# Performance work log

Measured on AMD Instinct MI355X. Metric: run time of the kernel, lower is better.

The kernel has to match this reference:

```python
import jax, jax.numpy as jnp
import numpy as np
from jax import lax

B, N, C = 8, 100000, 90
H = W = 512
CONF_THR = 0.25
IOU_THR = 0.45
MAX_DET = 100  # fixed-size padded replacement for dynamic per-image NMS output


def setup_inputs() -> dict:
    key = jax.random.key(0)
    k1, k2, k3, k4, k5 = jax.random.split(key, 5)
    # small deltas so exp(dw), exp(dh) stay sane
    regression = jax.random.normal(k1, (B, N, 4), jnp.float32) * 0.1
    # shifted logits so sigmoid scores are mostly below conf_threshold (realistic sparsity)
    classification = jax.random.normal(k2, (B, N, C), jnp.float32) * 2.0 - 4.0
    # anchors in (y1, x1, y2, x2), valid boxes inside a 512x512 canvas
    cy = jax.random.uniform(k3, (1, N), minval=0.0, maxval=float(H))
    cx = jax.random.uniform(k4, (1, N), minval=0.0, maxval=float(W))
    hw = jax.random.uniform(k5, (1, N, 2), minval=16.0, maxval=128.0)
    hh, ww = hw[..., 0], hw[..., 1]
    anchors = jnp.stack([cy - hh / 2, cx - ww / 2, cy + hh / 2, cx + ww / 2], axis=-1)
    imgs = jnp.zeros((B, 3, H, W), jnp.float32)  # only shape (H, W) is used
    return {"regression": regression, "classification": classification,
            "anchors": anchors, "imgs": imgs}


def _bbox_transform(anchors, regression):
    y_c_a = (anchors[..., 0] + anchors[..., 2]) / 2
    x_c_a = (anchors[..., 1] + anchors[..., 3]) / 2
    ha = anchors[..., 2] - anchors[..., 0]
    wa = anchors[..., 3] - anchors[..., 1]
    w = jnp.exp(regression[..., 3]) * wa
    h = jnp.exp(regression[..., 2]) * ha
    y_c = regression[..., 0] * ha + y_c_a
    x_c = regression[..., 1] * wa + x_c_a
    # output in (x1, y1, x2, y2)
    return jnp.stack([x_c - w / 2, y_c - h / 2, x_c + w / 2, y_c + h / 2], axis=-1)


def _clip_boxes(boxes, height, width):
    x = jnp.clip(boxes[..., 0::2], 0.0, float(width))
    y = jnp.clip(boxes[..., 1::2], 0.0, float(height))
    return jnp.stack([x[..., 0], y[..., 0], x[..., 1], y[..., 1]], axis=-1)


def _iou_one_vs_all(box, boxes):
    # box [4], boxes [N,4] in x1y1x2y2
    x1 = jnp.maximum(box[0], boxes[:, 0])
    y1 = jnp.maximum(box[1], boxes[:, 1])
    x2 = jnp.minimum(box[2], boxes[:, 2])
    y2 = jnp.minimum(box[3], boxes[:, 3])
    inter = jnp.clip(x2 - x1, 0.0) * jnp.clip(y2 - y1, 0.0)
    area = (box[2] - box[0]) * (box[3] - box[1])
    areas = (boxes[:, 2] - boxes[:, 0]) * (boxes[:, 3] - boxes[:, 1])
    return inter / (area + areas - inter + 1e-8)


def _process_image(boxes, cls_logits):
    # boxes [N,4], cls_logits [N,C]
    scores_all = jax.nn.sigmoid(cls_logits)
    max_scores = jnp.max(scores_all, axis=1)
    labels = jnp.argmax(scores_all, axis=1)
    # below-threshold anchors get -1 so they can never be selected (== torch pre-NMS filter)
    s0 = jnp.where(max_scores > CONF_THR, max_scores, -1.0)
    s0 = lax.stop_gradient(s0)
    boxes_sg = lax.stop_gradient(boxes)

    def step(sc, _):
        best = jnp.argmax(sc)
        valid = sc[best] > 0.0
        iou = _iou_one_vs_all(boxes_sg[best], boxes_sg)
        sc = jnp.where(valid & (iou > IOU_THR), -1.0, sc)
        sc = sc.at[best].set(-1.0)
        return sc, jnp.where(valid, best, -1)

    _, idx = lax.scan(step, s0, None, length=MAX_DET)  # [MAX_DET] int
    valid = idx >= 0
    idx_safe = jnp.maximum(idx, 0)
    out_scores = jnp.where(valid, max_scores[idx_safe], 0.0)
    out_labels = jnp.where(valid, labels[idx_safe], -1)
    out_boxes = jnp.where(valid[:, None], boxes[idx_safe], 0.0)
    return out_scores, out_labels, out_boxes


def reference(regression, classification, anchors, imgs):
    height, width = imgs.shape[2], imgs.shape[3]
    boxes = _bbox_transform(anchors, regression)          # [B,N,4]
    boxes = _clip_boxes(boxes, height, width)
    scores, labels, det_boxes = jax.vmap(_process_image)(boxes, classification)
    # padded outputs: scores [B,MAX_DET], labels [B,MAX_DET] (-1 = invalid), boxes [B,MAX_DET,4]
    return scores, labels, det_boxes
```

## Files before the change

### kernel.cpp

```cpp
#include <hip/hip_runtime.h>

#define NB 8
#define NA 100000
#define NC 90
#define MAXDET 100
#define KCAND 2048
#define NBINS 4096
#define NBLK 13
#define BLK_ANCH 8000
#define ABLK 64
#define MASK_WORDS 32
#define SROWS 504
#define CONF 0.25f
#define IOUT 0.45f

static constexpr size_t OFF_SCORE = 0;
static constexpr size_t OFF_LABEL = OFF_SCORE + (size_t)NB * NA * 4;
static constexpr size_t OFF_HROWS = OFF_LABEL + (size_t)NB * NA;
static constexpr size_t OFF_THR   = OFF_HROWS + (size_t)NB * NBLK * NBINS * 4;
static constexpr size_t OFF_CNT   = OFF_THR + 64;
static constexpr size_t OFF_CKEY  = OFF_CNT + 64;
static constexpr size_t OFF_SSC   = OFF_CKEY + (size_t)NB * KCAND * 8;
static constexpr size_t OFF_SLAB  = OFF_SSC + (size_t)NB * KCAND * 4;
static constexpr size_t OFF_SBOX  = OFF_SLAB + (size_t)NB * KCAND * 4;
static constexpr size_t OFF_MASK  = OFF_SBOX + (size_t)NB * KCAND * 16;

__device__ __forceinline__ float4 decode_clip(float4 a, float4 r) {
#pragma clang fp contract(off)
    float yca = (a.x + a.z) * 0.5f;
    float xca = (a.y + a.w) * 0.5f;
    float ha  = a.z - a.x;
    float wa  = a.w - a.y;
    float w   = expf(r.w) * wa;
    float h   = expf(r.z) * ha;
    float yc  = r.x * ha + yca;
    float xc  = r.y * wa + xca;
    float x1  = xc - w * 0.5f, y1 = yc - h * 0.5f;
    float x2  = xc + w * 0.5f, y2 = yc + h * 0.5f;
    x1 = fminf(fmaxf(x1, 0.0f), 512.0f);
    x2 = fminf(fmaxf(x2, 0.0f), 512.0f);
    y1 = fminf(fmaxf(y1, 0.0f), 512.0f);
    y2 = fminf(fmaxf(y2, 0.0f), 512.0f);
    return make_float4(x1, y1, x2, y2);
}

__global__ __launch_bounds__(256) void k_score_box(const float* __restrict__ cls,
                                                   float* __restrict__ ws_score,
                                                   unsigned char* __restrict__ ws_label) {
    __shared__ float tile[ABLK * NC];
    int t = threadIdx.x;
    const float4* g4 = (const float4*)(cls + (size_t)blockIdx.x * (ABLK * NC));
    float4* t4 = (float4*)tile;
#pragma unroll
    for (int i = t; i < ABLK * NC / 4; i += 256) t4[i] = g4[i];
    __syncthreads();

    int la = t >> 2, h = t & 3;
    int off = h * 22 + (h < 2 ? h : 2);
    int len = (h < 2) ? 23 : 22;
    const float* row = tile + la * NC + off;
    unsigned bord = 0u;
    int bci = 0;
    for (int i = 0; i < len; ++i) {
        unsigned u = __float_as_uint(row[i]);
        unsigned ord = u ^ (0x80000000u | (unsigned)((int)u >> 31));
        if (ord > bord) { bord = ord; bci = off + i; }
    }
    unsigned long long best =
        ((unsigned long long)bord << 32) | (unsigned long long)(unsigned)(NC - 1 - bci);
    unsigned long long o = __shfl_xor(best, 1, 64);
    if (o > best) best = o;
    o = __shfl_xor(best, 2, 64);
    if (o > best) best = o;
    if (h == 0) {
        int a = blockIdx.x * ABLK + la;
        unsigned ordv = (unsigned)(best >> 32);
        unsigned u = (ordv & 0x80000000u) ? (ordv ^ 0x80000000u) : ~ordv;
        float x = __uint_as_float(u);
        float s = 1.0f / (1.0f + expf(-x));
        ws_score[a] = s;
        ws_label[a] = (unsigned char)(NC - 1 - (unsigned)(best & 0xFFFFFFFFu));
    }
}

__global__ __launch_bounds__(256) void k_hist(const float* __restrict__ ws_score,
                                              unsigned* __restrict__ hrows) {
    __shared__ unsigned h[NBINS];
    int b = blockIdx.y, blk = blockIdx.x, tid = threadIdx.x;
    for (int i = tid; i < NBINS; i += 256) h[i] = 0u;
    __syncthreads();
    int base = blk * BLK_ANCH;
    int lim = min(BLK_ANCH, NA - base);
    const float* sc = ws_score + (size_t)b * NA + base;
    for (int i = tid; i < lim; i += 256) {
        float s = sc[i];
        if (s > CONF) {
            int bin = min((int)(s * (float)NBINS), NBINS - 1);
            atomicAdd(&h[bin], 1u);
        }
    }
    __syncthreads();
    unsigned* row = hrows + ((size_t)b * NBLK + blk) * NBINS;
    for (int i = tid; i < NBINS; i += 256) row[i] = h[i];
}

__global__ __launch_bounds__(256) void k_thresh(const unsigned* __restrict__ hrows,
                                                unsigned* __restrict__ thr_bin,
                                                unsigned* __restrict__ cnt) {
    __shared__ unsigned h[NBINS];
    __shared__ unsigned chunk[256];
    __shared__ int bstar;
    int b = blockIdx.x, t = threadIdx.x;
    for (int i = t; i < NBINS; i += 256) {
        unsigned s = 0;
        for (int r = 0; r < NBLK; ++r) s += hrows[((size_t)b * NBLK + r) * NBINS + i];
        h[i] = s;
    }
    if (t == 0) { bstar = NBINS - 1; cnt[b] = 0u; }
    __syncthreads();
    unsigned s = 0;
    for (int j = 0; j < 16; ++j) s += h[t * 16 + j];
    chunk[t] = s;
    __syncthreads();
    unsigned U = 0;
    for (int j = t + 1; j < 256; ++j) U += chunk[j];
    unsigned run = U;
    int cand = NBINS;
    for (int j = 15; j >= 0; --j) {
        run += h[t * 16 + j];
        if (run <= (unsigned)KCAND) cand = t * 16 + j;
    }
    if (cand < NBINS) atomicMin(&bstar, cand);
    __syncthreads();
    if (t == 0) thr_bin[b] = (unsigned)bstar;
}

__global__ __launch_bounds__(256) void k_compact(const float* __restrict__ ws_score,
                                                 const unsigned* __restrict__ thr_bin,
                                                 unsigned* __restrict__ cnt,
                                                 unsigned long long* __restrict__ ckey) {
    __shared__ unsigned scan[256];
    __shared__ unsigned base_s;
    int b = blockIdx.y, blk = blockIdx.x, t = threadIdx.x;
    int base = blk * BLK_ANCH;
    int lim = min(BLK_ANCH, NA - base);
    size_t ibase = (size_t)b * NA + base;
    unsigned thr = thr_bin[b];

    unsigned c = 0;
    for (int i = t; i < lim; i += 256) {
        float s = ws_score[ibase + i];
        if (s > CONF) {
            int bin = min((int)(s * (float)NBINS), NBINS - 1);
            if ((unsigned)bin >= thr) c++;
        }
    }
    scan[t] = c;
    __syncthreads();
    for (int off = 1; off < 256; off <<= 1) {
        unsigned v = (t >= off) ? scan[t - off] : 0u;
        __syncthreads();
        scan[t] += v;
        __syncthreads();
    }
    if (t == 255) base_s = atomicAdd(&cnt[b], scan[255]);
    __syncthreads();
    unsigned pos = base_s + scan[t] - c;
    for (int i = t; i < lim; i += 256) {
        float s = ws_score[ibase + i];
        if (s > CONF) {
            int bin = min((int)(s * (float)NBINS), NBINS - 1);
            if ((unsigned)bin >= thr) {
                unsigned p = pos++;
                if (p < (unsigned)KCAND) {
                    int n = base + i;
                    ckey[(size_t)b * KCAND + p] =
                        ((unsigned long long)__float_as_uint(s) << 32) |
                        (unsigned long long)(0xFFFFFFFFu - (unsigned)n);
                }
            }
        }
    }
}

__global__ __launch_bounds__(1024) void k_sortdecode(const unsigned long long* __restrict__ ckey,
                                                     const unsigned* __restrict__ cnt,
                                                     const unsigned char* __restrict__ ws_label,
                                                     const float* __restrict__ reg,
                                                     const float* __restrict__ anc,
                                                     float* __restrict__ sscore,
                                                     int* __restrict__ slab,
                                                     float4* __restrict__ sbox) {
    __shared__ unsigned long long key[KCAND];
    int b = blockIdx.x, t = threadIdx.x;
    unsigned M = min(cnt[b], (unsigned)KCAND);
    for (int i = t; i < KCAND; i += 1024)
        key[i] = (i < (int)M) ? ckey[(size_t)b * KCAND + i] : 0ULL;
    __syncthreads();
    for (int k = 2; k <= KCAND; k <<= 1) {
        for (int j = k >> 1; j > 0; j >>= 1) {
#pragma unroll
            for (int s = 0; s < KCAND / 1024; ++s) {
                int p = t + s * 1024;
                int q = p ^ j;
                if (q > p) {
                    unsigned long long a = key[p], bb = key[q];
                    bool desc = ((p & k) == 0);
                    if (desc ? (a < bb) : (a > bb)) { key[p] = bb; key[q] = a; }
                }
            }
            __syncthreads();
        }
    }
    for (int i = t; i < KCAND; i += 1024) {
        unsigned long long kk = key[i];
        size_t o = (size_t)b * KCAND + i;
        if (kk != 0ULL) {
            unsigned n = 0xFFFFFFFFu - (unsigned)(kk & 0xFFFFFFFFu);
            sscore[o] = __uint_as_float((unsigned)(kk >> 32));
            slab[o] = (int)ws_label[(size_t)b * NA + n];
            float4 a4 = ((const float4*)anc)[n];
            float4 r4 = ((const float4*)reg)[(size_t)b * NA + n];
            sbox[o] = decode_clip(a4, r4);
        } else {
            sscore[o] = 0.0f;
            slab[o] = -1;
            sbox[o] = make_float4(0.f, 0.f, 0.f, 0.f);
        }
    }
}

__global__ __launch_bounds__(256) void k_mask(const float4* __restrict__ sbox,
                                              unsigned long long* __restrict__ mask) {
    __shared__ float4 bx[KCAND];
    int b = blockIdx.y, t = threadIdx.x;
    for (int i = t; i < KCAND; i += 256) bx[i] = sbox[(size_t)b * KCAND + i];
    __syncthreads();
    int r = t >> 5, w = t & 31;
    int row = blockIdx.x * 8 + r;
    float4 rb = bx[row];
    unsigned long long bits = 0ULL;
    {
#pragma clang fp contract(off)
        float areaR = (rb.z - rb.x) * (rb.w - rb.y);
        int cbase = w * 64;
        for (int cc = 0; cc < 64; ++cc) {
            float4 cb = bx[cbase + cc];
            float x1 = fmaxf(rb.x, cb.x), y1 = fmaxf(rb.y, cb.y);
            float x2 = fminf(rb.z, cb.z), y2 = fminf(rb.w, cb.w);
            float inter = fmaxf(x2 - x1, 0.0f) * fmaxf(y2 - y1, 0.0f);
            float areaC = (cb.z - cb.x) * (cb.w - cb.y);
            float iou = inter / (areaR + areaC - inter + 1e-8f);
            if (iou > IOUT) bits |= (1ULL << cc);
        }
    }
    mask[((size_t)b * KCAND + row) * MASK_WORDS + w] = bits;
}

__global__ __launch_bounds__(256) void k_scan(const unsigned long long* __restrict__ mask,
                                              const unsigned* __restrict__ cnt,
                                              const float* __restrict__ sscore,
                                              const int* __restrict__ slab,
                                              const float4* __restrict__ sbox,
                                              float* __restrict__ out) {
    __shared__ unsigned long long lmask[SROWS * MASK_WORDS];
    __shared__ int picks[MAXDET];
    __shared__ int np_s;
    int b = blockIdx.x, t = threadIdx.x;
    const unsigned long long* mb = mask + (size_t)b * KCAND * MASK_WORDS;

    float4* l4 = (float4*)lmask;
    const float4* m4 = (const float4*)mb;
    for (int i = t; i < SROWS * MASK_WORDS / 2; i += 256) l4[i] = m4[i];
    __syncthreads();

    if (t < 64) {
        int l = t;
        unsigned M = min(cnt[b], (unsigned)KCAND);
        unsigned long long valid = 0ULL;
        if (l < 32) {
            int rem = (int)M - l * 64;
            valid = (rem >= 64) ? ~0ULL : ((rem > 0) ? ((1ULL << rem) - 1ULL) : 0ULL);
        }
        unsigned long long removed = 0ULL;
        int np = 0;
        while (np < MAXDET) {
            unsigned long long free_ = valid & ~removed;
            unsigned long long act = __ballot(free_ != 0ULL);
            if (act == 0ULL) break;
            int lstar = __ffsll((long long)act) - 1;
            unsigned long long fw = __shfl(free_, lstar, 64);
            int bit = __ffsll((long long)fw) - 1;
            int c = lstar * 64 + bit;
            if (l == 0) picks[np] = c;
            np++;
            if (l == lstar) removed |= (1ULL << bit);
            if (l < 32) {
                unsigned long long rw;
                if (c < SROWS) rw = lmask[c * MASK_WORDS + l];
                else rw = mb[(size_t)c * MASK_WORDS + l];
                removed |= rw;
            }
        }
        if (l == 0) np_s = np;
    }
    __syncthreads();

    int np = np_s;
    for (int k = t; k < MAXDET; k += 256) {
        float sc = 0.0f, lb = -1.0f;
        float4 bb = make_float4(0.f, 0.f, 0.f, 0.f);
        if (k < np) {
            int i = picks[k];
            size_t o = (size_t)b * KCAND + i;
            sc = sscore[o];
            lb = (float)slab[o];
            bb = sbox[o];
        }
        out[b * MAXDET + k] = sc;
        out[NB * MAXDET + b * MAXDET + k] = lb;
        ((float4*)(out + 2 * NB * MAXDET))[b * MAXDET + k] = bb;
    }
}

extern "C" void kernel_launch(void* const* d_in, const int* in_sizes, int n_in,
                              void* d_out, int out_size, void* d_ws, size_t ws_size,
                              hipStream_t stream) {
    const float* reg = (const float*)d_in[0];
    const float* cls = (const float*)d_in[1];
    const float* anc = (const float*)d_in[2];

    char* ws = (char*)d_ws;
    float* ws_score           = (float*)(ws + OFF_SCORE);
    unsigned char* ws_label   = (unsigned char*)(ws + OFF_LABEL);
    unsigned* hrows           = (unsigned*)(ws + OFF_HROWS);
    unsigned* thr_bin         = (unsigned*)(ws + OFF_THR);
    unsigned* cnt             = (unsigned*)(ws + OFF_CNT);
    unsigned long long* ckey  = (unsigned long long*)(ws + OFF_CKEY);
    float* sscore             = (float*)(ws + OFF_SSC);
    int* slab                 = (int*)(ws + OFF_SLAB);
    float4* sbox              = (float4*)(ws + OFF_SBOX);
    unsigned long long* maskp = (unsigned long long*)(ws + OFF_MASK);

    float* out = (float*)d_out;

    k_score_box<<<NB * NA / ABLK, 256, 0, stream>>>(cls, ws_score, ws_label);
    k_hist<<<dim3(NBLK, NB), 256, 0, stream>>>(ws_score, hrows);
    k_thresh<<<NB, 256, 0, stream>>>(hrows, thr_bin, cnt);
    k_compact<<<dim3(NBLK, NB), 256, 0, stream>>>(ws_score, thr_bin, cnt, ckey);
    k_sortdecode<<<NB, 1024, 0, stream>>>(ckey, cnt, ws_label, reg, anc, sscore, slab, sbox);
    k_mask<<<dim3(KCAND / 8, NB), 256, 0, stream>>>(sbox, maskp);
    k_scan<<<NB, 256, 0, stream>>>(maskp, cnt, sscore, slab, sbox, out);
}
```

Before: 566.3 us.

## Fuse histogram, threshold and compaction into one per-image select kernel; skip lower-triangle mask

Replaces the three kernels for histogram, threshold and compaction with a single 1024-thread block per image. That block builds the histogram in shared memory, finds the threshold bin and compacts candidates in order without global atomics. This removes two launches and the global histogram round-trip, but the pass over 100k scores is now done by only 8 blocks. The mask kernel also remaps threads so each row skips 64-column words that lie entirely below the diagonal, and it rotates the column start to spread LDS bank accesses. Skipped words are written as zero, which assumes the scan only reads bits above the diagonal.

```diff
diff --git a/kernel.cpp b/kernel.cpp
--- a/kernel.cpp
+++ b/kernel.cpp
@@ -6,8 +6,6 @@
 #define MAXDET 100
 #define KCAND 2048
 #define NBINS 4096
-#define NBLK 13
-#define BLK_ANCH 8000
 #define ABLK 64
 #define MASK_WORDS 32
 #define SROWS 504
@@ -16,8 +14,7 @@
 
 static constexpr size_t OFF_SCORE = 0;
 static constexpr size_t OFF_LABEL = OFF_SCORE + (size_t)NB * NA * 4;
-static constexpr size_t OFF_HROWS = OFF_LABEL + (size_t)NB * NA;
-static constexpr size_t OFF_THR   = OFF_HROWS + (size_t)NB * NBLK * NBINS * 4;
+static constexpr size_t OFF_THR   = OFF_LABEL + (size_t)NB * NA;
 static constexpr size_t OFF_CNT   = OFF_THR + 64;
 static constexpr size_t OFF_CKEY  = OFF_CNT + 64;
 static constexpr size_t OFF_SSC   = OFF_CKEY + (size_t)NB * KCAND * 8;
@@ -83,104 +80,78 @@
     }
 }
 
-__global__ __launch_bounds__(256) void k_hist(const float* __restrict__ ws_score,
-                                              unsigned* __restrict__ hrows) {
-    __shared__ unsigned h[NBINS];
-    int b = blockIdx.y, blk = blockIdx.x, tid = threadIdx.x;
-    for (int i = tid; i < NBINS; i += 256) h[i] = 0u;
-    __syncthreads();
-    int base = blk * BLK_ANCH;
-    int lim = min(BLK_ANCH, NA - base);
-    const float* sc = ws_score + (size_t)b * NA + base;
-    for (int i = tid; i < lim; i += 256) {
+__global__ __launch_bounds__(1024) void k_select(const float* __restrict__ ws_score,
+                                                 unsigned* __restrict__ cnt,
+                                                 unsigned long long* __restrict__ ckey) {
+    __shared__ unsigned hist[NBINS];
+    __shared__ unsigned chunk[256];
+    __shared__ unsigned sscan[1024];
+    __shared__ int bstar;
+    int b = blockIdx.x, t = threadIdx.x;
+    const float* sc = ws_score + (size_t)b * NA;
+
+    for (int i = t; i < NBINS; i += 1024) hist[i] = 0u;
+    if (t == 0) bstar = NBINS - 1;
+    __syncthreads();
+    for (int i = t; i < NA; i += 1024) {
         float s = sc[i];
         if (s > CONF) {
             int bin = min((int)(s * (float)NBINS), NBINS - 1);
-            atomicAdd(&h[bin], 1u);
-        }
-    }
-    __syncthreads();
-    unsigned* row = hrows + ((size_t)b * NBLK + blk) * NBINS;
-    for (int i = tid; i < NBINS; i += 256) row[i] = h[i];
-}
-
-__global__ __launch_bounds__(256) void k_thresh(const unsigned* __restrict__ hrows,
-                                                unsigned* __restrict__ thr_bin,
-                                                unsigned* __restrict__ cnt) {
-    __shared__ unsigned h[NBINS];
-    __shared__ unsigned chunk[256];
-    __shared__ int bstar;
-    int b = blockIdx.x, t = threadIdx.x;
-    for (int i = t; i < NBINS; i += 256) {
+            atomicAdd(&hist[bin], 1u);
+        }
+    }
+    __syncthreads();
+    if (t < 256) {
         unsigned s = 0;
-        for (int r = 0; r < NBLK; ++r) s += hrows[((size_t)b * NBLK + r) * NBINS + i];
-        h[i] = s;
-    }
-    if (t == 0) { bstar = NBINS - 1; cnt[b] = 0u; }
-    __syncthreads();
-    unsigned s = 0;
-    for (int j = 0; j < 16; ++j) s += h[t * 16 + j];
-    chunk[t] = s;
-    __syncthreads();
-    unsigned U = 0;
-    for (int j = t + 1; j < 256; ++j) U += chunk[j];
-    unsigned run = U;
-    int cand = NBINS;
-    for (int j = 15; j >= 0; --j) {
-        run += h[t * 16 + j];
-        if (run <= (unsigned)KCAND) cand = t * 16 + j;
-    }
-    if (cand < NBINS) atomicMin(&bstar, cand);
-    __syncthreads();
-    if (t == 0) thr_bin[b] = (unsigned)bstar;
-}
-
-__global__ __launch_bounds__(256) void k_compact(const float* __restrict__ ws_score,
-                                                 const unsigned* __restrict__ thr_bin,
-                                                 unsigned* __restrict__ cnt,
-                                                 unsigned long long* __restrict__ ckey) {
-    __shared__ unsigned scan[256];
-    __shared__ unsigned base_s;
-    int b = blockIdx.y, blk = blockIdx.x, t = threadIdx.x;
-    int base = blk * BLK_ANCH;
-    int lim = min(BLK_ANCH, NA - base);
-    size_t ibase = (size_t)b * NA + base;
-    unsigned thr = thr_bin[b];
+        for (int j = 0; j < 16; ++j) s += hist[t * 16 + j];
+        chunk[t] = s;
+    }
+    __syncthreads();
+    if (t < 256) {
+        unsigned U = 0;
+        for (int j = t + 1; j < 256; ++j) U += chunk[j];
+        unsigned run = U;
+        int cand = NBINS;
+        for (int j = 15; j >= 0; --j) {
+            run += hist[t * 16 + j];
+            if (run <= (unsigned)KCAND) cand = t * 16 + j;
+        }
+        if (cand < NBINS) atomicMin(&bstar, cand);
+    }
+    __syncthreads();
+    unsigned thr = (unsigned)bstar;
 
     unsigned c = 0;
-    for (int i = t; i < lim; i += 256) {
-        float s = ws_score[ibase + i];
+    for (int i = t; i < NA; i += 1024) {
+        float s = sc[i];
         if (s > CONF) {
             int bin = min((int)(s * (float)NBINS), NBINS - 1);
             if ((unsigned)bin >= thr) c++;
         }
     }
-    scan[t] = c;
-    __syncthreads();
-    for (int off = 1; off < 256; off <<= 1) {
-        unsigned v = (t >= off) ? scan[t - off] : 0u;
+    sscan[t] = c;
+    __syncthreads();
+    for (int off = 1; off < 1024; off <<= 1) {
+        unsigned v = (t >= off) ? sscan[t - off] : 0u;
         __syncthreads();
-        scan[t] += v;
+        sscan[t] += v;
         __syncthreads();
     }
-    if (t == 255) base_s = atomicAdd(&cnt[b], scan[255]);
-    __syncthreads();
-    unsigned pos = base_s + scan[t] - c;
-    for (int i = t; i < lim; i += 256) {
-        float s = ws_score[ibase + i];
+    unsigned pos = sscan[t] - c;
+    for (int i = t; i < NA; i += 1024) {
+        float s = sc[i];
         if (s > CONF) {
             int bin = min((int)(s * (float)NBINS), NBINS - 1);
             if ((unsigned)bin >= thr) {
                 unsigned p = pos++;
-                if (p < (unsigned)KCAND) {
-                    int n = base + i;
+                if (p < (unsigned)KCAND)
                     ckey[(size_t)b * KCAND + p] =
                         ((unsigned long long)__float_as_uint(s) << 32) |
-                        (unsigned long long)(0xFFFFFFFFu - (unsigned)n);
-                }
+                        (unsigned long long)(0xFFFFFFFFu - (unsigned)i);
             }
         }
     }
+    if (t == 1023) cnt[b] = sscan[1023];
 }
 
 __global__ __launch_bounds__(1024) void k_sortdecode(const unsigned long long* __restrict__ ckey,
@@ -236,15 +207,16 @@
     int b = blockIdx.y, t = threadIdx.x;
     for (int i = t; i < KCAND; i += 256) bx[i] = sbox[(size_t)b * KCAND + i];
     __syncthreads();
-    int r = t >> 5, w = t & 31;
+    int r = t & 7, w = t >> 3;
     int row = blockIdx.x * 8 + r;
-    float4 rb = bx[row];
+    int cbase = w * 64;
     unsigned long long bits = 0ULL;
-    {
+    if (cbase + 63 >= row) {
 #pragma clang fp contract(off)
+        float4 rb = bx[row];
         float areaR = (rb.z - rb.x) * (rb.w - rb.y);
-        int cbase = w * 64;
-        for (int cc = 0; cc < 64; ++cc) {
+        for (int k = 0; k < 64; ++k) {
+            int cc = (k + w) & 63;
             float4 cb = bx[cbase + cc];
             float x1 = fmaxf(rb.x, cb.x), y1 = fmaxf(rb.y, cb.y);
             float x2 = fminf(rb.z, cb.z), y2 = fminf(rb.w, cb.w);
@@ -333,8 +305,6 @@
     char* ws = (char*)d_ws;
     float* ws_score           = (float*)(ws + OFF_SCORE);
     unsigned char* ws_label   = (unsigned char*)(ws + OFF_LABEL);
-    unsigned* hrows           = (unsigned*)(ws + OFF_HROWS);
-    unsigned* thr_bin         = (unsigned*)(ws + OFF_THR);
     unsigned* cnt             = (unsigned*)(ws + OFF_CNT);
     unsigned long long* ckey  = (unsigned long long*)(ws + OFF_CKEY);
     float* sscore             = (float*)(ws + OFF_SSC);
@@ -345,9 +315,7 @@
     float* out = (float*)d_out;
 
     k_score_box<<<NB * NA / ABLK, 256, 0, stream>>>(cls, ws_score, ws_label);
-    k_hist<<<dim3(NBLK, NB), 256, 0, stream>>>(ws_score, hrows);
-    k_thresh<<<NB, 256, 0, stream>>>(hrows, thr_bin, cnt);
-    k_compact<<<dim3(NBLK, NB), 256, 0, stream>>>(ws_score, thr_bin, cnt, ckey);
+    k_select<<<NB, 1024, 0, stream>>>(ws_score, cnt, ckey);
     k_sortdecode<<<NB, 1024, 0, stream>>>(ckey, cnt, ws_label, reg, anc, sscore, slab, sbox);
     k_mask<<<dim3(KCAND / 8, NB), 256, 0, stream>>>(sbox, maskp);
     k_scan<<<NB, 256, 0, stream>>>(maskp, cnt, sscore, slab, sbox, out);
```

After: 564.9 us. Within noise of the previous version (-0.3%).
